# Kernel optimization log

Measured on AMD Instinct MI355X. Metric: run time of the kernel, lower is better.

## Reference

```python
import jax, jax.numpy as jnp
import numpy as np

B, S, D, H, HID, NUM_POS = 8, 512, 512, 8, 2048, 1
DIM = D // H
EPS = 1e-3  # keras LayerNormalization default epsilon


def _ln(x, g, b):
    mu = jnp.mean(x, axis=-1, keepdims=True)
    var = jnp.mean(jnp.square(x - mu), axis=-1, keepdims=True)
    return (x - mu) * jax.lax.rsqrt(var + EPS) * g + b


def setup_inputs() -> dict:
    key = jax.random.key(0)
    ks = jax.random.split(key, 12)
    s = 0.02
    return {
        "values": jax.random.normal(ks[0], (B, S, D), jnp.float32),
        "values_mask": jnp.ones((B, S), jnp.bool_),
        "ln0_g": jnp.ones((D,), jnp.float32),
        "ln0_b": jnp.zeros((D,), jnp.float32),
        "W0a": jax.random.normal(ks[1], (D, HID), jnp.float32) * s,
        "b0a": jnp.zeros((HID,), jnp.float32),
        "W0b": jax.random.normal(ks[2], (HID, 3 * D), jnp.float32) * s,
        "b0b": jnp.zeros((3 * D,), jnp.float32),
        "Wp": jax.random.normal(ks[3], (2 * NUM_POS + 1, D), jnp.float32) * s,
        "bp": jnp.zeros((D,), jnp.float32),
        "ln1_g": jnp.ones((D,), jnp.float32),
        "ln1_b": jnp.zeros((D,), jnp.float32),
        "W1a": jax.random.normal(ks[4], (D, HID), jnp.float32) * s,
        "b1a": jnp.zeros((HID,), jnp.float32),
        "W1b": jax.random.normal(ks[5], (HID, D), jnp.float32) * s,
        "b1b": jnp.zeros((D,), jnp.float32),
    }


def reference(values, values_mask, ln0_g, ln0_b, W0a, b0a, W0b, b0b,
              Wp, bp, ln1_g, ln1_b, W1a, b1a, W1b, b1b):
    # Block0: LN -> Dense(HID, relu) -> Dense(3D)  (QKV projection)
    h = _ln(values, ln0_g, ln0_b)
    x = jax.nn.relu(h @ W0a + b0a) @ W0b + b0b            # [B,S,3D]
    x = x.reshape(B, S, H, 3 * DIM).transpose(0, 2, 1, 3)  # [B,H,S,3*dim]
    q, k, v = x[..., :DIM], x[..., DIM:2 * DIM], x[..., 2 * DIM:]

    # relative positions (l2r identity permutation): one-hot(clip(j-i)) @ Wp + bp
    idx = jnp.clip(jnp.arange(S)[None, :] - jnp.arange(S)[:, None],
                   -NUM_POS, NUM_POS) + NUM_POS            # [S,S] in {0,1,2}
    pos = Wp[idx] + bp                                     # [S,S,D]
    pos = pos.reshape(S, S, H, DIM).transpose(2, 0, 1, 3)  # [H,S,S,dim]

    # bias_{bhqk} = q_{bhqd} . pos_{hqkd}
    bias = jnp.einsum('bhqd,hqkd->bhqk', q, pos)

    scores = bias + jnp.einsum('bhqd,bhkd->bhqk', q, k) / jnp.sqrt(
        jnp.asarray(DIM, jnp.float32))

    mask = values_mask[:, None, :, None] & values_mask[:, None, None, :]
    causal = jnp.tril(jnp.ones((S, S), jnp.bool_))
    mask = mask & causal[None, None]
    att = jax.nn.softmax(jnp.where(mask, scores, -999999.0), axis=-1)

    o = jnp.einsum('bhqk,bhkd->bhqd', att, v)              # [B,H,S,dim]
    o = o.transpose(0, 2, 1, 3).reshape(B, S, D)
    values = values + o

    # Block1 FFN residual
    h = _ln(values, ln1_g, ln1_b)
    values = values + (jax.nn.relu(h @ W1a + b1a) @ W1b + b1b)
    return values
```

## Files before the change

kernel.cpp:

```cpp
#include <hip/hip_runtime.h>
#include <hip/hip_bf16.h>
#include <stdint.h>

using hbf = __hip_bfloat16;
typedef __bf16 bf16x8 __attribute__((ext_vector_type(8)));
typedef float f32x4 __attribute__((ext_vector_type(4)));

#define MFMA16(a, b, c) __builtin_amdgcn_mfma_f32_16x16x32_bf16((a), (b), (c), 0, 0, 0)

__device__ __forceinline__ void async_copy16(const void* gsrc, void* ldst) {
  __builtin_amdgcn_global_load_lds((const __attribute__((address_space(1))) void*)gsrc,
                                   (__attribute__((address_space(3))) void*)ldst,
                                   16, 0, 0);
}

__global__ __launch_bounds__(256) void wtrans_all(const float* __restrict__ W0a,
                                                  const float* __restrict__ W0b,
                                                  const float* __restrict__ W1a,
                                                  const float* __restrict__ W1b,
                                                  hbf* __restrict__ T0a, hbf* __restrict__ T0b,
                                                  hbf* __restrict__ T1a, hbf* __restrict__ T1b) {
  __shared__ float tile[64][65];
  const int idx = blockIdx.x;
  const float* W; hbf* Wt; int K, N, nt, i;
  if (idx < 256)        { W = W0a; Wt = T0a; K = 512;  N = 2048; nt = 32; i = idx; }
  else if (idx < 1024)  { W = W0b; Wt = T0b; K = 2048; N = 1536; nt = 24; i = idx - 256; }
  else if (idx < 1280)  { W = W1a; Wt = T1a; K = 512;  N = 2048; nt = 32; i = idx - 1024; }
  else                  { W = W1b; Wt = T1b; K = 2048; N = 512;  nt = 8;  i = idx - 1280; }
  const int n0 = (i % nt) * 64, k0 = (i / nt) * 64;
  const int tid = threadIdx.x;
#pragma unroll
  for (int t = 0; t < 16; ++t) {
    int q = tid + t * 256;
    int r = q >> 6, c = q & 63;
    tile[r][c] = W[(size_t)(k0 + r) * N + n0 + c];
  }
  __syncthreads();
#pragma unroll
  for (int t = 0; t < 16; ++t) {
    int q = tid + t * 256;
    int r = q >> 6, c = q & 63;
    Wt[(size_t)(n0 + r) * K + k0 + c] = __float2bfloat16(tile[c][r]);
  }
}

__global__ __launch_bounds__(256) void ln0_kernel(const float* __restrict__ x,
                                                  const float* __restrict__ g,
                                                  const float* __restrict__ bt,
                                                  hbf* __restrict__ h) {
  const int row = blockIdx.x * 4 + (threadIdx.x >> 6);
  const int l = threadIdx.x & 63;
  const float* xr = x + (size_t)row * 512;
  float v[8], s = 0.f, s2 = 0.f;
#pragma unroll
  for (int i = 0; i < 8; ++i) {
    float t = xr[l + 64 * i];
    v[i] = t; s += t; s2 += t * t;
  }
#pragma unroll
  for (int off = 32; off; off >>= 1) { s += __shfl_xor(s, off); s2 += __shfl_xor(s2, off); }
  float mu = s * (1.f / 512.f);
  float rs = rsqrtf(s2 * (1.f / 512.f) - mu * mu + 1e-3f);
  hbf* hr = h + (size_t)row * 512;
#pragma unroll
  for (int i = 0; i < 8; ++i) {
    int c = l + 64 * i;
    hr[c] = __float2bfloat16((v[i] - mu) * rs * g[c] + bt[c]);
  }
}

__global__ __launch_bounds__(256) void lnadd_kernel(const float* __restrict__ values,
                                                    const float* __restrict__ obuf,
                                                    const float* __restrict__ g,
                                                    const float* __restrict__ bt,
                                                    float* __restrict__ res1,
                                                    hbf* __restrict__ h2) {
  const int row = blockIdx.x * 4 + (threadIdx.x >> 6);
  const int l = threadIdx.x & 63;
  const float* vr = values + (size_t)row * 512;
  const float* orow = obuf + (size_t)row * 512;
  float* rr = res1 + (size_t)row * 512;
  float v[8], s = 0.f, s2 = 0.f;
#pragma unroll
  for (int i = 0; i < 8; ++i) {
    int c = l + 64 * i;
    float t = vr[c] + orow[c];
    v[i] = t; s += t; s2 += t * t;
    rr[c] = t;
  }
#pragma unroll
  for (int off = 32; off; off >>= 1) { s += __shfl_xor(s, off); s2 += __shfl_xor(s2, off); }
  float mu = s * (1.f / 512.f);
  float rs = rsqrtf(s2 * (1.f / 512.f) - mu * mu + 1e-3f);
  hbf* hr = h2 + (size_t)row * 512;
#pragma unroll
  for (int i = 0; i < 8; ++i) {
    int c = l + 64 * i;
    hr[c] = __float2bfloat16((v[i] - mu) * rs * g[c] + bt[c]);
  }
}

template <int EPI, int BN>
__global__ __launch_bounds__(256) void gemm_bt(const hbf* __restrict__ A,
                                               const hbf* __restrict__ Bt,
                                               const float* __restrict__ bias,
                                               const float* __restrict__ resid,
                                               void* __restrict__ outp,
                                               int M, int N, int K) {
  constexpr int WCOLS = (BN == 64) ? 2 : 1;
  constexpr int WROWS = 4 / WCOLS;
  constexpr int MI = 128 / (WROWS * 16);
  constexpr int NJ = BN / (WCOLS * 16);
  constexpr int BCH = BN / 32;
  __shared__ hbf As[2][128 * 64];
  __shared__ hbf Bs[2][BN * 64];
  const int tid = threadIdx.x;
  const int lane = tid & 63;
  const int w = tid >> 6;
  const int wm = w / WCOLS, wn = w % WCOLS;

  const int nbx = gridDim.x;
  const int nwg = nbx * gridDim.y;
  const int bid = blockIdx.y * nbx + blockIdx.x;
  const int cpx = nwg >> 3;
  const int sw = (bid & 7) * cpx + (bid >> 3);
  const int m0 = (sw / nbx) * 128, n0 = (sw % nbx) * BN;

  f32x4 acc[MI][NJ] = {};

  int ar[4], ac[4];
#pragma unroll
  for (int p = 0; p < 4; ++p) {
    int off = p * 4096 + tid * 16;
    int r = off >> 7, sl = (off >> 4) & 7;
    ar[p] = r;
    ac[p] = sl ^ (r & 7);
  }

  auto stage = [&](int buf, int kt) {
#pragma unroll
    for (int p = 0; p < 4; ++p)
      async_copy16(A + (size_t)(m0 + ar[p]) * K + kt + ac[p] * 8,
                   (char*)As[buf] + p * 4096 + tid * 16);
#pragma unroll
    for (int p = 0; p < BCH; ++p)
      async_copy16(Bt + (size_t)(n0 + ar[p]) * K + kt + ac[p] * 8,
                   (char*)Bs[buf] + p * 4096 + tid * 16);
  };

  stage(0, 0);
  __syncthreads();
  int cur = 0;

  for (int kt = 0; kt < K; kt += 64) {
    if (kt + 64 < K) stage(cur ^ 1, kt + 64);
    const int cq = lane >> 4, lr = lane & 15;
    bf16x8 af[2][MI], bg[2][NJ];
#pragma unroll
    for (int i = 0; i < MI; ++i) {
      int m = wm * (MI * 16) + i * 16 + lr;
#pragma unroll
      for (int kk = 0; kk < 2; ++kk) {
        int sl = (kk * 4 + cq) ^ (m & 7);
        af[kk][i] = *reinterpret_cast<const bf16x8*>((const char*)As[cur] + m * 128 + sl * 16);
      }
    }
#pragma unroll
    for (int j = 0; j < NJ; ++j) {
      int n = wn * (NJ * 16) + j * 16 + lr;
#pragma unroll
      for (int kk = 0; kk < 2; ++kk) {
        int sl = (kk * 4 + cq) ^ (n & 7);
        bg[kk][j] = *reinterpret_cast<const bf16x8*>((const char*)Bs[cur] + n * 128 + sl * 16);
      }
    }
#pragma unroll
    for (int kk = 0; kk < 2; ++kk)
#pragma unroll
      for (int i = 0; i < MI; ++i)
#pragma unroll
        for (int j = 0; j < NJ; ++j)
          acc[i][j] = MFMA16(af[kk][i], bg[kk][j], acc[i][j]);
    __syncthreads();
    cur ^= 1;
  }

#pragma unroll
  for (int j = 0; j < NJ; ++j) {
    int col = n0 + wn * (NJ * 16) + j * 16 + (lane & 15);
    float bcol = bias[col];
#pragma unroll
    for (int i = 0; i < MI; ++i) {
      int rowb = m0 + wm * (MI * 16) + i * 16 + (lane >> 4) * 4;
#pragma unroll
      for (int r = 0; r < 4; ++r) {
        int row = rowb + r;
        float v = acc[i][j][r] + bcol;
        if (EPI == 0) {
          v = v > 0.f ? v : 0.f;
          ((hbf*)outp)[(size_t)row * N + col] = __float2bfloat16(v);
        } else if (EPI == 1) {
          ((hbf*)outp)[(size_t)row * N + col] = __float2bfloat16(v);
        } else {
          ((float*)outp)[(size_t)row * N + col] = v + resid[(size_t)row * N + col];
        }
      }
    }
  }
}

__global__ __launch_bounds__(256) void vtrans_kernel(const hbf* __restrict__ X2,
                                                     hbf* __restrict__ vT) {
  __shared__ hbf tile[64][80];
  const int bh = blockIdx.x, s0 = blockIdx.y * 64;
  const int b = bh >> 3, h = bh & 7;
  const int tid = threadIdx.x;
#pragma unroll
  for (int i = 0; i < 2; ++i) {
    int chunk = tid + i * 256;
    int r = chunk >> 3, c8 = (chunk & 7) * 8;
    const hbf* src = X2 + (size_t)(b * 512 + s0 + r) * 1536 + h * 192 + 128 + c8;
    *reinterpret_cast<bf16x8*>(&tile[r][c8]) = *reinterpret_cast<const bf16x8*>(src);
  }
  __syncthreads();
#pragma unroll
  for (int i = 0; i < 2; ++i) {
    int chunk = tid + i * 256;
    int d = chunk >> 3, s8 = (chunk & 7) * 8;
    bf16x8 v;
#pragma unroll
    for (int j = 0; j < 8; ++j) v[j] = *reinterpret_cast<const __bf16*>(&tile[s8 + j][d]);
    *reinterpret_cast<bf16x8*>(vT + ((size_t)bh * 64 + d) * 512 + s0 + s8) = v;
  }
}

__global__ __launch_bounds__(256) void posbias_kernel(const hbf* __restrict__ X2,
                                                      const float* __restrict__ Wp,
                                                      const float* __restrict__ bp,
                                                      float* __restrict__ bb) {
  int idx = blockIdx.x * 256 + threadIdx.x;
  int c = idx >> 15;
  int r = idx & 32767;
  int bh = r >> 9, q = r & 511;
  int b = bh >> 3, h = bh & 7;
  const hbf* qp = X2 + (size_t)(b * 512 + q) * 1536 + h * 192;
  const float* wr = Wp + c * 512 + h * 64;
  const float* br = bp + h * 64;
  float s = 0.f;
#pragma unroll
  for (int d8 = 0; d8 < 8; ++d8) {
    bf16x8 qv = *reinterpret_cast<const bf16x8*>(qp + d8 * 8);
#pragma unroll
    for (int j = 0; j < 8; ++j) s += (float)qv[j] * (wr[d8 * 8 + j] + br[d8 * 8 + j]);
  }
  bb[idx] = s;
}

__global__ __launch_bounds__(256) void attn_kernel(const hbf* __restrict__ X2,
                                                   const hbf* __restrict__ vT,
                                                   const float* __restrict__ bb,
                                                   float* __restrict__ obuf) {
  __shared__ hbf p_lds[4][16][32];
  const int bh = blockIdx.x;
  const int b = bh >> 3, h = bh & 7;
  const int q0 = blockIdx.y * 64;
  const int tid = threadIdx.x;
  const int lane = tid & 63, w = tid >> 6;
  const int qbase = q0 + w * 16;

  bf16x8 qa[2];
  {
    int qrow = qbase + (lane & 15);
    const hbf* qp = X2 + (size_t)(b * 512 + qrow) * 1536 + h * 192 + (lane >> 4) * 8;
#pragma unroll
    for (int c = 0; c < 2; ++c) qa[c] = *reinterpret_cast<const bf16x8*>(qp + c * 32);
  }
  float bias0[4], bias1[4];
#pragma unroll
  for (int r = 0; r < 4; ++r) {
    int qr = qbase + (lane >> 4) * 4 + r;
    bias0[r] = bb[bh * 512 + qr];
    bias1[r] = bb[32768 + bh * 512 + qr];
  }

  float mrow[4], lsum[4];
  f32x4 oacc[4];
#pragma unroll
  for (int r = 0; r < 4; ++r) { mrow[r] = -1e30f; lsum[r] = 0.f; }
#pragma unroll
  for (int nt = 0; nt < 4; ++nt) oacc[nt] = (f32x4){0.f, 0.f, 0.f, 0.f};

  const int qhi = qbase + 15;
  const int nchunks = (qhi >> 5) + 1;
  for (int ch = 0; ch < nchunks; ++ch) {
    const int k32 = ch * 32;
    f32x4 z = {0.f, 0.f, 0.f, 0.f};
    f32x4 s0, s1;
    {
      const hbf* kp = X2 + (size_t)(b * 512 + k32 + (lane & 15)) * 1536 + h * 192 + 64 + (lane >> 4) * 8;
      bf16x8 kb = *reinterpret_cast<const bf16x8*>(kp);
      s0 = MFMA16(qa[0], kb, z);
      kb = *reinterpret_cast<const bf16x8*>(kp + 32);
      s0 = MFMA16(qa[1], kb, s0);
      const hbf* kp1 = kp + 16 * 1536;
      kb = *reinterpret_cast<const bf16x8*>(kp1);
      s1 = MFMA16(qa[0], kb, z);
      kb = *reinterpret_cast<const bf16x8*>(kp1 + 32);
      s1 = MFMA16(qa[1], kb, s1);
    }
    const int col0 = k32 + (lane & 15);
    const int col1 = col0 + 16;
    float p0[4], p1[4], alpha[4];
#pragma unroll
    for (int r = 0; r < 4; ++r) {
      int q = qbase + (lane >> 4) * 4 + r;
      float sc0 = (col0 > q) ? -1e30f : (s0[r] * 0.125f + (col0 == q ? bias1[r] : bias0[r]));
      float sc1 = (col1 > q) ? -1e30f : (s1[r] * 0.125f + (col1 == q ? bias1[r] : bias0[r]));
      float cm = fmaxf(sc0, sc1);
#pragma unroll
      for (int off = 1; off < 16; off <<= 1) cm = fmaxf(cm, __shfl_xor(cm, off));
      float mn = fmaxf(mrow[r], cm);
      alpha[r] = __expf(mrow[r] - mn);
      mrow[r] = mn;
      float e0 = __expf(sc0 - mn), e1 = __expf(sc1 - mn);
      p0[r] = e0; p1[r] = e1;
      float ps = e0 + e1;
#pragma unroll
      for (int off = 1; off < 16; off <<= 1) ps += __shfl_xor(ps, off);
      lsum[r] = lsum[r] * alpha[r] + ps;
    }
#pragma unroll
    for (int nt = 0; nt < 4; ++nt)
#pragma unroll
      for (int r = 0; r < 4; ++r) oacc[nt][r] *= alpha[r];
#pragma unroll
    for (int r = 0; r < 4; ++r) {
      p_lds[w][(lane >> 4) * 4 + r][lane & 15] = __float2bfloat16(p0[r]);
      p_lds[w][(lane >> 4) * 4 + r][16 + (lane & 15)] = __float2bfloat16(p1[r]);
    }
    bf16x8 pa = *reinterpret_cast<const bf16x8*>(&p_lds[w][lane & 15][(lane >> 4) * 8]);
#pragma unroll
    for (int nt = 0; nt < 4; ++nt) {
      const hbf* vp = vT + ((size_t)bh * 64 + nt * 16 + (lane & 15)) * 512 + k32 + (lane >> 4) * 8;
      bf16x8 vb = *reinterpret_cast<const bf16x8*>(vp);
      oacc[nt] = MFMA16(pa, vb, oacc[nt]);
    }
  }
#pragma unroll
  for (int r = 0; r < 4; ++r) {
    float rl = 1.f / lsum[r];
    int q = qbase + (lane >> 4) * 4 + r;
    float* orow = obuf + (size_t)(b * 512 + q) * 512 + h * 64;
#pragma unroll
    for (int nt = 0; nt < 4; ++nt) orow[nt * 16 + (lane & 15)] = oacc[nt][r] * rl;
  }
}

extern "C" void kernel_launch(void* const* d_in, const int* in_sizes, int n_in,
                              void* d_out, int out_size, void* d_ws, size_t ws_size,
                              hipStream_t stream) {
  const float* values = (const float*)d_in[0];
  const float* ln0_g = (const float*)d_in[2];
  const float* ln0_b = (const float*)d_in[3];
  const float* W0a = (const float*)d_in[4];
  const float* b0a = (const float*)d_in[5];
  const float* W0b = (const float*)d_in[6];
  const float* b0b = (const float*)d_in[7];
  const float* Wp = (const float*)d_in[8];
  const float* bp = (const float*)d_in[9];
  const float* ln1_g = (const float*)d_in[10];
  const float* ln1_b = (const float*)d_in[11];
  const float* W1a = (const float*)d_in[12];
  const float* b1a = (const float*)d_in[13];
  const float* W1b = (const float*)d_in[14];
  const float* b1b = (const float*)d_in[15];

  char* ws = (char*)d_ws;
  hbf* W0a_t = (hbf*)(ws + (0ull << 20));
  hbf* W0b_t = (hbf*)(ws + (2ull << 20));
  hbf* W1a_t = (hbf*)(ws + (8ull << 20));
  hbf* W1b_t = (hbf*)(ws + (10ull << 20));
  hbf* hbuf = (hbf*)(ws + (12ull << 20));
  hbf* X1 = (hbf*)(ws + (16ull << 20));
  hbf* X2 = (hbf*)(ws + (32ull << 20));
  float* obuf = (float*)(ws + (44ull << 20));
  hbf* vT = (hbf*)(ws + (52ull << 20));
  float* bb = (float*)(ws + (56ull << 20));
  float* res1 = (float*)(ws + (57ull << 20));
  hbf* X3 = X1;
  hbf* h2 = hbuf;

  wtrans_all<<<1536, 256, 0, stream>>>(W0a, W0b, W1a, W1b, W0a_t, W0b_t, W1a_t, W1b_t);

  ln0_kernel<<<1024, 256, 0, stream>>>(values, ln0_g, ln0_b, hbuf);

  gemm_bt<0, 64><<<dim3(32, 32), 256, 0, stream>>>(hbuf, W0a_t, b0a, nullptr, X1, 4096, 2048, 512);
  gemm_bt<1, 64><<<dim3(24, 32), 256, 0, stream>>>(X1, W0b_t, b0b, nullptr, X2, 4096, 1536, 2048);

  vtrans_kernel<<<dim3(64, 8), 256, 0, stream>>>(X2, vT);
  posbias_kernel<<<256, 256, 0, stream>>>(X2, Wp, bp, bb);
  attn_kernel<<<dim3(64, 8), 256, 0, stream>>>(X2, vT, bb, obuf);

  lnadd_kernel<<<1024, 256, 0, stream>>>(values, obuf, ln1_g, ln1_b, res1, h2);

  gemm_bt<0, 64><<<dim3(32, 32), 256, 0, stream>>>(h2, W1a_t, b1a, nullptr, X3, 4096, 2048, 512);
  gemm_bt<2, 32><<<dim3(16, 32), 256, 0, stream>>>(X3, W1b_t, b1b, res1, (float*)d_out, 4096, 512, 2048);
}
```

Baseline: 232.3 us.

## Merge small prep kernels and relax GEMM pipeline waits with explicit vmcnt barriers

Fuses the weight-transpose and LN0 kernels into one launch, and the V-transpose and positional-bias kernels into another, so two kernel launches and their boundaries go away. In the GEMM main loop, the blanket __syncthreads is replaced with explicit s_waitcnt vmcnt counts plus raw barriers. The next tile's async loads can then stay in flight while the current tile is consumed. The hand-tuned vmcnt values depend on how many loads each stage issues, so they are fragile if the tile shape changes.

```diff
diff --git a/kernel.cpp b/kernel.cpp
--- a/kernel.cpp
+++ b/kernel.cpp
@@ -14,21 +14,47 @@
                                    16, 0, 0);
 }
 
-__global__ __launch_bounds__(256) void wtrans_all(const float* __restrict__ W0a,
-                                                  const float* __restrict__ W0b,
-                                                  const float* __restrict__ W1a,
-                                                  const float* __restrict__ W1b,
-                                                  hbf* __restrict__ T0a, hbf* __restrict__ T0b,
-                                                  hbf* __restrict__ T1a, hbf* __restrict__ T1b) {
+__global__ __launch_bounds__(256) void prep_kernel(const float* __restrict__ W0a,
+                                                   const float* __restrict__ W0b,
+                                                   const float* __restrict__ W1a,
+                                                   const float* __restrict__ W1b,
+                                                   hbf* __restrict__ T0a, hbf* __restrict__ T0b,
+                                                   hbf* __restrict__ T1a, hbf* __restrict__ T1b,
+                                                   const float* __restrict__ x,
+                                                   const float* __restrict__ g,
+                                                   const float* __restrict__ bt,
+                                                   hbf* __restrict__ h) {
+  const int idx = blockIdx.x;
+  const int tid = threadIdx.x;
+  if (idx >= 1536) {
+    const int row = (idx - 1536) * 4 + (tid >> 6);
+    const int l = tid & 63;
+    const float* xr = x + (size_t)row * 512;
+    float v[8], s = 0.f, s2 = 0.f;
+#pragma unroll
+    for (int i = 0; i < 8; ++i) {
+      float t = xr[l + 64 * i];
+      v[i] = t; s += t; s2 += t * t;
+    }
+#pragma unroll
+    for (int off = 32; off; off >>= 1) { s += __shfl_xor(s, off); s2 += __shfl_xor(s2, off); }
+    float mu = s * (1.f / 512.f);
+    float rs = rsqrtf(s2 * (1.f / 512.f) - mu * mu + 1e-3f);
+    hbf* hr = h + (size_t)row * 512;
+#pragma unroll
+    for (int i = 0; i < 8; ++i) {
+      int c = l + 64 * i;
+      hr[c] = __float2bfloat16((v[i] - mu) * rs * g[c] + bt[c]);
+    }
+    return;
+  }
   __shared__ float tile[64][65];
-  const int idx = blockIdx.x;
   const float* W; hbf* Wt; int K, N, nt, i;
   if (idx < 256)        { W = W0a; Wt = T0a; K = 512;  N = 2048; nt = 32; i = idx; }
   else if (idx < 1024)  { W = W0b; Wt = T0b; K = 2048; N = 1536; nt = 24; i = idx - 256; }
   else if (idx < 1280)  { W = W1a; Wt = T1a; K = 512;  N = 2048; nt = 32; i = idx - 1024; }
   else                  { W = W1b; Wt = T1b; K = 2048; N = 512;  nt = 8;  i = idx - 1280; }
   const int n0 = (i % nt) * 64, k0 = (i / nt) * 64;
-  const int tid = threadIdx.x;
 #pragma unroll
   for (int t = 0; t < 16; ++t) {
     int q = tid + t * 256;
@@ -41,31 +67,6 @@
     int q = tid + t * 256;
     int r = q >> 6, c = q & 63;
     Wt[(size_t)(n0 + r) * K + k0 + c] = __float2bfloat16(tile[c][r]);
-  }
-}
-
-__global__ __launch_bounds__(256) void ln0_kernel(const float* __restrict__ x,
-                                                  const float* __restrict__ g,
-                                                  const float* __restrict__ bt,
-                                                  hbf* __restrict__ h) {
-  const int row = blockIdx.x * 4 + (threadIdx.x >> 6);
-  const int l = threadIdx.x & 63;
-  const float* xr = x + (size_t)row * 512;
-  float v[8], s = 0.f, s2 = 0.f;
-#pragma unroll
-  for (int i = 0; i < 8; ++i) {
-    float t = xr[l + 64 * i];
-    v[i] = t; s += t; s2 += t * t;
-  }
-#pragma unroll
-  for (int off = 32; off; off >>= 1) { s += __shfl_xor(s, off); s2 += __shfl_xor(s2, off); }
-  float mu = s * (1.f / 512.f);
-  float rs = rsqrtf(s2 * (1.f / 512.f) - mu * mu + 1e-3f);
-  hbf* hr = h + (size_t)row * 512;
-#pragma unroll
-  for (int i = 0; i < 8; ++i) {
-    int c = l + 64 * i;
-    hr[c] = __float2bfloat16((v[i] - mu) * rs * g[c] + bt[c]);
   }
 }
 
@@ -149,11 +150,19 @@
   };
 
   stage(0, 0);
-  __syncthreads();
   int cur = 0;
 
   for (int kt = 0; kt < K; kt += 64) {
-    if (kt + 64 < K) stage(cur ^ 1, kt + 64);
+    if (kt + 64 < K) {
+      stage(cur ^ 1, kt + 64);
+      if constexpr (BN == 64) asm volatile("s_waitcnt vmcnt(6)" ::: "memory");
+      else                    asm volatile("s_waitcnt vmcnt(5)" ::: "memory");
+    } else {
+      asm volatile("s_waitcnt vmcnt(0)" ::: "memory");
+    }
+    __builtin_amdgcn_s_barrier();
+    __builtin_amdgcn_sched_barrier(0);
+
     const int cq = lane >> 4, lr = lane & 15;
     bf16x8 af[2][MI], bg[2][NJ];
 #pragma unroll
@@ -181,7 +190,9 @@
 #pragma unroll
         for (int j = 0; j < NJ; ++j)
           acc[i][j] = MFMA16(af[kk][i], bg[kk][j], acc[i][j]);
-    __syncthreads();
+
+    __builtin_amdgcn_sched_barrier(0);
+    __builtin_amdgcn_s_barrier();
     cur ^= 1;
   }
 
@@ -209,36 +220,37 @@
   }
 }
 
-__global__ __launch_bounds__(256) void vtrans_kernel(const hbf* __restrict__ X2,
-                                                     hbf* __restrict__ vT) {
-  __shared__ hbf tile[64][80];
-  const int bh = blockIdx.x, s0 = blockIdx.y * 64;
-  const int b = bh >> 3, h = bh & 7;
-  const int tid = threadIdx.x;
-#pragma unroll
-  for (int i = 0; i < 2; ++i) {
-    int chunk = tid + i * 256;
-    int r = chunk >> 3, c8 = (chunk & 7) * 8;
-    const hbf* src = X2 + (size_t)(b * 512 + s0 + r) * 1536 + h * 192 + 128 + c8;
-    *reinterpret_cast<bf16x8*>(&tile[r][c8]) = *reinterpret_cast<const bf16x8*>(src);
-  }
-  __syncthreads();
-#pragma unroll
-  for (int i = 0; i < 2; ++i) {
-    int chunk = tid + i * 256;
-    int d = chunk >> 3, s8 = (chunk & 7) * 8;
-    bf16x8 v;
-#pragma unroll
-    for (int j = 0; j < 8; ++j) v[j] = *reinterpret_cast<const __bf16*>(&tile[s8 + j][d]);
-    *reinterpret_cast<bf16x8*>(vT + ((size_t)bh * 64 + d) * 512 + s0 + s8) = v;
-  }
-}
-
-__global__ __launch_bounds__(256) void posbias_kernel(const hbf* __restrict__ X2,
+__global__ __launch_bounds__(256) void postqkv_kernel(const hbf* __restrict__ X2,
+                                                      hbf* __restrict__ vT,
                                                       const float* __restrict__ Wp,
                                                       const float* __restrict__ bp,
                                                       float* __restrict__ bb) {
-  int idx = blockIdx.x * 256 + threadIdx.x;
+  const int blk = blockIdx.x;
+  const int tid = threadIdx.x;
+  if (blk < 512) {
+    __shared__ hbf tile[64][80];
+    const int bh = blk >> 3, s0 = (blk & 7) * 64;
+    const int b = bh >> 3, h = bh & 7;
+#pragma unroll
+    for (int i = 0; i < 2; ++i) {
+      int chunk = tid + i * 256;
+      int r = chunk >> 3, c8 = (chunk & 7) * 8;
+      const hbf* src = X2 + (size_t)(b * 512 + s0 + r) * 1536 + h * 192 + 128 + c8;
+      *reinterpret_cast<bf16x8*>(&tile[r][c8]) = *reinterpret_cast<const bf16x8*>(src);
+    }
+    __syncthreads();
+#pragma unroll
+    for (int i = 0; i < 2; ++i) {
+      int chunk = tid + i * 256;
+      int d = chunk >> 3, s8 = (chunk & 7) * 8;
+      bf16x8 v;
+#pragma unroll
+      for (int j = 0; j < 8; ++j) v[j] = *reinterpret_cast<const __bf16*>(&tile[s8 + j][d]);
+      *reinterpret_cast<bf16x8*>(vT + ((size_t)bh * 64 + d) * 512 + s0 + s8) = v;
+    }
+    return;
+  }
+  int idx = (blk - 512) * 256 + tid;
   int c = idx >> 15;
   int r = idx & 32767;
   int bh = r >> 9, q = r & 511;
@@ -390,15 +402,13 @@
   hbf* X3 = X1;
   hbf* h2 = hbuf;
 
-  wtrans_all<<<1536, 256, 0, stream>>>(W0a, W0b, W1a, W1b, W0a_t, W0b_t, W1a_t, W1b_t);
-
-  ln0_kernel<<<1024, 256, 0, stream>>>(values, ln0_g, ln0_b, hbuf);
+  prep_kernel<<<2560, 256, 0, stream>>>(W0a, W0b, W1a, W1b, W0a_t, W0b_t, W1a_t, W1b_t,
+                                        values, ln0_g, ln0_b, hbuf);
 
   gemm_bt<0, 64><<<dim3(32, 32), 256, 0, stream>>>(hbuf, W0a_t, b0a, nullptr, X1, 4096, 2048, 512);
   gemm_bt<1, 64><<<dim3(24, 32), 256, 0, stream>>>(X1, W0b_t, b0b, nullptr, X2, 4096, 1536, 2048);
 
-  vtrans_kernel<<<dim3(64, 8), 256, 0, stream>>>(X2, vT);
-  posbias_kernel<<<256, 256, 0, stream>>>(X2, Wp, bp, bb);
+  postqkv_kernel<<<768, 256, 0, stream>>>(X2, vT, Wp, bp, bb);
   attn_kernel<<<dim3(64, 8), 256, 0, stream>>>(X2, vT, bb, obuf);
 
   lnadd_kernel<<<1024, 256, 0, stream>>>(values, obuf, ln1_g, ln1_b, res1, h2);
```

Measured after the change: 230.9 us. About the same (-0.6%).
